# Optimization experiments

Measured on AMD Instinct MI355X. Metric: run time of the kernel, lower is better.

## Reference

```python
import jax, jax.numpy as jnp
import numpy as np
import math

B, S, D, H = 4, 2048, 512, 8
HD = D // H  # head dim = 64

def setup_inputs() -> dict:
    key = jax.random.key(0)
    ks = jax.random.split(key, 12)
    inp = {
        'queries': jax.random.normal(ks[0], (B, S, D), jnp.float32),
        'keys': jax.random.normal(ks[1], (B, S, D), jnp.float32),
        'values': jax.random.normal(ks[2], (B, S, D), jnp.float32),
        'valid_lens': jax.random.randint(ks[3], (B,), 0, 2048, jnp.int32),
        'Wq': jax.random.normal(ks[4], (D, D), jnp.float32) / math.sqrt(D),
        'bq': jnp.zeros((D,), jnp.float32),
        'Wk': jax.random.normal(ks[5], (D, D), jnp.float32) / math.sqrt(D),
        'bk': jnp.zeros((D,), jnp.float32),
        'Wv': jax.random.normal(ks[6], (D, D), jnp.float32) / math.sqrt(D),
        'bv': jnp.zeros((D,), jnp.float32),
        'Wo': jax.random.normal(ks[7], (D, D), jnp.float32) / math.sqrt(D),
        'bo': jnp.zeros((D,), jnp.float32),
    }
    return inp

def reference(queries, keys, values, valid_lens, Wq, bq, Wk, bk, Wv, bv, Wo, bo):
    # project and split heads: [B,S,D] -> [B,H,S,HD]
    def split_heads(x):
        return x.reshape(B, S, H, HD).transpose(0, 2, 1, 3)
    q = split_heads(queries @ Wq + bq)
    k = split_heads(keys @ Wk + bk)
    v = split_heads(values @ Wv + bv)
    # scores [B,H,Sq,Sk]
    scores = jnp.einsum('bhqd,bhkd->bhqk', q, k) / math.sqrt(HD)
    # masked softmax: mask key positions >= valid_len with -1e6 (d2l semantics)
    mask = jnp.arange(S)[None, None, None, :] < valid_lens[:, None, None, None]
    scores = jnp.where(mask, scores, -1e6)
    attn = jax.nn.softmax(scores, axis=-1)
    out = jnp.einsum('bhqk,bhkd->bhqd', attn, v)  # [B,H,S,HD]
    out = out.transpose(0, 2, 1, 3).reshape(B, S, D)
    return out @ Wo + bo
```

## Files before the change

### kernel.cpp

```cpp
#include <hip/hip_runtime.h>
#include <hip/hip_bf16.h>

typedef _Float16 half8 __attribute__((ext_vector_type(8)));
typedef _Float16 half4 __attribute__((ext_vector_type(4)));
typedef float floatx4 __attribute__((ext_vector_type(4)));

#define LOG2E 1.44269504088896340736f

__device__ __forceinline__ half8 cvt8r(floatx4 a, floatx4 b) {
    half8 h;
    h[0] = (_Float16)a[0]; h[1] = (_Float16)a[1]; h[2] = (_Float16)a[2]; h[3] = (_Float16)a[3];
    h[4] = (_Float16)b[0]; h[5] = (_Float16)b[1]; h[6] = (_Float16)b[2]; h[7] = (_Float16)b[3];
    return h;
}

__global__ __launch_bounds__(256) void transpose_w_kernel(
        const float* __restrict__ Wq, const float* __restrict__ Wk,
        const float* __restrict__ Wv, const float* __restrict__ Wo,
        _Float16* __restrict__ out) {
    const float* W = (blockIdx.z == 0) ? Wq : (blockIdx.z == 1) ? Wk : (blockIdx.z == 2) ? Wv : Wo;
    _Float16* o = out + (size_t)blockIdx.z * 512 * 512;
    __shared__ __align__(16) _Float16 t[64][72];
    int r0 = blockIdx.x * 64, c0 = blockIdx.y * 64;
    int tid = threadIdx.x;
    for (int i = 0; i < 2; i++) {
        int f = i * 256 + tid;
        int row = f >> 3, seg = f & 7;
        const float* p = W + (size_t)(r0 + row) * 512 + c0 + seg * 8;
        *(half8*)&t[row][seg * 8] = cvt8r(*(const floatx4*)p, *(const floatx4*)(p + 4));
    }
    __syncthreads();
    for (int i = 0; i < 2; i++) {
        int f = i * 256 + tid;
        int crow = f >> 3, seg = f & 7;
        half8 hv;
        for (int j = 0; j < 8; j++) hv[j] = t[seg * 8 + j][crow];
        *(half8*)(o + (size_t)(c0 + crow) * 512 + r0 + seg * 8) = hv;
    }
}

__global__ __launch_bounds__(256) void gemm_qkv_kernel(
        const float* __restrict__ Xq, const float* __restrict__ Xk, const float* __restrict__ Xv,
        const _Float16* __restrict__ WTall,
        const float* __restrict__ bq, const float* __restrict__ bk, const float* __restrict__ bv,
        _Float16* __restrict__ qo, _Float16* __restrict__ ko2, _Float16* __restrict__ vto) {
    int z = blockIdx.z;
    const float* X = (z == 0) ? Xq : (z == 1) ? Xk : Xv;
    const _Float16* BT = WTall + (size_t)z * 512 * 512;
    const float* bias = (z == 0) ? bq : (z == 1) ? bk : bv;

    __shared__ __align__(16) _Float16 Asm[128][72];
    __shared__ __align__(16) _Float16 Bsm[128][72];

    int tid = threadIdx.x;
    int wave = tid >> 6, lane = tid & 63;
    int lrow = lane & 15, quad = lane >> 4;
    int m0 = (wave >> 1) * 64, n0 = (wave & 1) * 64;
    int mBase = blockIdx.x * 128, nBase = blockIdx.y * 128;

    const floatx4 fz = {0.f, 0.f, 0.f, 0.f};
    floatx4 acc[4][4];
    for (int i = 0; i < 4; i++) for (int j = 0; j < 4; j++) acc[i][j] = fz;

    floatx4 areg[4][2];
    half8 breg[4];
    int srow[4], sseg[4];
    for (int i = 0; i < 4; i++) { int f = i * 256 + tid; srow[i] = f >> 3; sseg[i] = f & 7; }

    for (int i = 0; i < 4; i++) {
        const float* pa = X + (size_t)(mBase + srow[i]) * 512 + sseg[i] * 8;
        areg[i][0] = *(const floatx4*)pa;
        areg[i][1] = *(const floatx4*)(pa + 4);
        breg[i] = *(const half8*)(BT + (size_t)(nBase + srow[i]) * 512 + sseg[i] * 8);
    }

    for (int kb = 0; kb < 512; kb += 64) {
        for (int i = 0; i < 4; i++) {
            *(half8*)&Asm[srow[i]][sseg[i] * 8] = cvt8r(areg[i][0], areg[i][1]);
            *(half8*)&Bsm[srow[i]][sseg[i] * 8] = breg[i];
        }
        __syncthreads();
        if (kb + 64 < 512) {
            int kn = kb + 64;
            for (int i = 0; i < 4; i++) {
                const float* pa = X + (size_t)(mBase + srow[i]) * 512 + kn + sseg[i] * 8;
                areg[i][0] = *(const floatx4*)pa;
                areg[i][1] = *(const floatx4*)(pa + 4);
                breg[i] = *(const half8*)(BT + (size_t)(nBase + srow[i]) * 512 + kn + sseg[i] * 8);
            }
        }
        for (int kc = 0; kc < 2; kc++) {
            int ko_ = kc * 32 + quad * 8;
            half8 a[4], b[4];
            for (int mt = 0; mt < 4; mt++) a[mt] = *(const half8*)&Asm[m0 + mt * 16 + lrow][ko_];
            for (int nt = 0; nt < 4; nt++) b[nt] = *(const half8*)&Bsm[n0 + nt * 16 + lrow][ko_];
            for (int mt = 0; mt < 4; mt++)
                for (int nt = 0; nt < 4; nt++)
                    acc[mt][nt] = __builtin_amdgcn_mfma_f32_16x16x32_f16(a[mt], b[nt], acc[mt][nt], 0, 0, 0);
        }
        __syncthreads();
    }

    if (z == 2) {
        for (int nt = 0; nt < 4; nt++) {
            int gc = nBase + n0 + nt * 16 + lrow;
            float bb = bias[gc];
            int h = gc >> 6, hd = gc & 63;
            for (int mt = 0; mt < 4; mt++) {
                int gr = mBase + m0 + mt * 16 + quad * 4;
                int b_ = gr >> 11, s = gr & 2047;
                half4 hv;
                for (int r = 0; r < 4; r++) hv[r] = (_Float16)(acc[mt][nt][r] + bb);
                *(half4*)(vto + (((size_t)(b_ * 8 + h) * 64 + hd) * 2048 + s)) = hv;
            }
        }
    } else {
        _Float16* out = (z == 0) ? qo : ko2;
        for (int nt = 0; nt < 4; nt++) {
            int gc = nBase + n0 + nt * 16 + lrow;
            float bb = bias[gc];
            int h = gc >> 6, hd = gc & 63;
            for (int mt = 0; mt < 4; mt++) {
                for (int r = 0; r < 4; r++) {
                    int gr = mBase + m0 + mt * 16 + quad * 4 + r;
                    int b_ = gr >> 11, s = gr & 2047;
                    out[(((size_t)b_ * 8 + h) * 2048 + s) * 64 + hd] = (_Float16)(acc[mt][nt][r] + bb);
                }
            }
        }
    }
}

__global__ __launch_bounds__(256) void attn_kernel(
        const _Float16* __restrict__ qws, const _Float16* __restrict__ kws, const _Float16* __restrict__ vtws,
        const int* __restrict__ vlens, _Float16* __restrict__ aout) {
    int idx = blockIdx.x;
    int b = ((idx & 3) + (idx >> 8)) & 3;
    int h = (idx >> 2) & 7;
    int q0 = ((idx >> 5) & 31) * 64;
    int bh = b * 8 + h;
    int L = vlens[b];
    bool uni = (L == 0);
    int nkt = uni ? 32 : ((L + 63) >> 6);
    int tid = threadIdx.x;
    int wave = tid >> 6, lane = tid & 63;
    int lrow = lane & 15, quad = lane >> 4;

    __shared__ __align__(16) _Float16 ksm[64][72];
    __shared__ __align__(16) _Float16 vtsm[80][72];

    for (int i = tid; i < 15 * 36; i += 256) {
        int r = i / 36, c = i % 36;
        ((float*)&vtsm[65 + r][0])[c] = 0.0f;
    }
    if (tid < 64) vtsm[64][tid] = (_Float16)1.0f;

    const _Float16* qbase = qws + ((size_t)bh * 2048 + q0) * 64;
    const _Float16* kbase = kws + (size_t)bh * 2048 * 64;
    const _Float16* vtbase = vtws + (size_t)bh * 64 * 2048;

    half8 qf[2];
    for (int kc = 0; kc < 2; kc++) {
        qf[kc] = *(const half8*)(qbase + (wave * 16 + lrow) * 64 + kc * 32 + quad * 8);
        qf[kc] = qf[kc] * (_Float16)(0.125f * LOG2E);
    }

    const floatx4 fz = {0.f, 0.f, 0.f, 0.f};
    floatx4 oacc[5];
    for (int nt = 0; nt < 5; nt++) oacc[nt] = fz;

    int row0 = tid >> 3, seg = tid & 7;
    half8 kreg[2], vreg[2];
    {
        const _Float16* kt0 = kbase;
        const _Float16* vt0 = vtbase;
        kreg[0] = *(const half8*)(kt0 + tid * 8);
        kreg[1] = *(const half8*)(kt0 + (256 + tid) * 8);
        vreg[0] = *(const half8*)(vt0 + (size_t)row0 * 2048 + seg * 8);
        vreg[1] = *(const half8*)(vt0 + (size_t)(row0 + 32) * 2048 + seg * 8);
    }

    for (int kt = 0; kt < nkt; kt++) {
        *(half8*)&ksm[row0][seg * 8]        = kreg[0];
        *(half8*)&ksm[row0 + 32][seg * 8]   = kreg[1];
        *(half8*)&vtsm[row0][seg * 8]       = vreg[0];
        *(half8*)&vtsm[row0 + 32][seg * 8]  = vreg[1];
        __syncthreads();

        if (kt + 1 < nkt) {
            const _Float16* ktn = kbase + (size_t)(kt + 1) * 64 * 64;
            const _Float16* vtn = vtbase + (kt + 1) * 64;
            kreg[0] = *(const half8*)(ktn + tid * 8);
            kreg[1] = *(const half8*)(ktn + (256 + tid) * 8);
            vreg[0] = *(const half8*)(vtn + (size_t)row0 * 2048 + seg * 8);
            vreg[1] = *(const half8*)(vtn + (size_t)(row0 + 32) * 2048 + seg * 8);
        }

        floatx4 sacc[4];
        for (int km = 0; km < 4; km++) sacc[km] = fz;
        for (int kc = 0; kc < 2; kc++) {
            int ko_ = kc * 32 + quad * 8;
            for (int km = 0; km < 4; km++) {
                half8 kf = *(const half8*)&ksm[km * 16 + lrow][ko_];
                sacc[km] = __builtin_amdgcn_mfma_f32_16x16x32_f16(kf, qf[kc], sacc[km], 0, 0, 0);
            }
        }

        half4 pf[4];
        int kb0 = kt * 64 + quad * 4;
        for (int km = 0; km < 4; km++) {
            int kb = kb0 + km * 16;
            for (int r = 0; r < 4; r++) {
                float p = uni ? 1.0f : ((kb + r < L) ? exp2f(sacc[km][r]) : 0.0f);
                pf[km][r] = (_Float16)p;
            }
        }

        for (int km = 0; km < 4; km++) {
            int kk = km * 16 + quad * 4;
            for (int nt = 0; nt < 5; nt++) {
                half4 bvf = *(const half4*)&vtsm[nt * 16 + lrow][kk];
                oacc[nt] = __builtin_amdgcn_mfma_f32_16x16x16f16(pf[km], bvf, oacc[nt], 0, 0, 0);
            }
        }
        __syncthreads();
    }

    float inv[4];
    for (int r = 0; r < 4; r++)
        inv[r] = 1.0f / __shfl(oacc[4][r], quad << 4, 64);

    for (int nt = 0; nt < 4; nt++) {
        for (int r = 0; r < 4; r++) {
            int s = q0 + wave * 16 + quad * 4 + r;
            aout[((size_t)b * 2048 + s) * 512 + h * 64 + nt * 16 + lrow] =
                (_Float16)(oacc[nt][r] * inv[r]);
        }
    }
}

__global__ __launch_bounds__(256) void gemm_out_kernel(
        const _Float16* __restrict__ A, const _Float16* __restrict__ BT,
        const float* __restrict__ bias, float* __restrict__ out) {
    __shared__ __align__(16) _Float16 Asm[128][72];
    __shared__ __align__(16) _Float16 Bsm[128][72];

    int tid = threadIdx.x;
    int wave = tid >> 6, lane = tid & 63;
    int lrow = lane & 15, quad = lane >> 4;
    int m0 = (wave >> 1) * 64, n0 = (wave & 1) * 64;
    int mBase = blockIdx.x * 128, nBase = blockIdx.y * 128;

    const floatx4 fz = {0.f, 0.f, 0.f, 0.f};
    floatx4 acc[4][4];
    for (int i = 0; i < 4; i++) for (int j = 0; j < 4; j++) acc[i][j] = fz;

    half8 areg[4], breg[4];
    int srow[4], sseg[4];
    for (int i = 0; i < 4; i++) { int f = i * 256 + tid; srow[i] = f >> 3; sseg[i] = f & 7; }
    for (int i = 0; i < 4; i++) {
        areg[i] = *(const half8*)(A + (size_t)(mBase + srow[i]) * 512 + sseg[i] * 8);
        breg[i] = *(const half8*)(BT + (size_t)(nBase + srow[i]) * 512 + sseg[i] * 8);
    }

    for (int kb = 0; kb < 512; kb += 64) {
        for (int i = 0; i < 4; i++) {
            *(half8*)&Asm[srow[i]][sseg[i] * 8] = areg[i];
            *(half8*)&Bsm[srow[i]][sseg[i] * 8] = breg[i];
        }
        __syncthreads();
        if (kb + 64 < 512) {
            int kn = kb + 64;
            for (int i = 0; i < 4; i++) {
                areg[i] = *(const half8*)(A + (size_t)(mBase + srow[i]) * 512 + kn + sseg[i] * 8);
                breg[i] = *(const half8*)(BT + (size_t)(nBase + srow[i]) * 512 + kn + sseg[i] * 8);
            }
        }
        for (int kc = 0; kc < 2; kc++) {
            int ko_ = kc * 32 + quad * 8;
            half8 a[4], b[4];
            for (int mt = 0; mt < 4; mt++) a[mt] = *(const half8*)&Asm[m0 + mt * 16 + lrow][ko_];
            for (int nt = 0; nt < 4; nt++) b[nt] = *(const half8*)&Bsm[n0 + nt * 16 + lrow][ko_];
            for (int mt = 0; mt < 4; mt++)
                for (int nt = 0; nt < 4; nt++)
                    acc[mt][nt] = __builtin_amdgcn_mfma_f32_16x16x32_f16(a[mt], b[nt], acc[mt][nt], 0, 0, 0);
        }
        __syncthreads();
    }

    for (int nt = 0; nt < 4; nt++) {
        int gc = nBase + n0 + nt * 16 + lrow;
        float bb = bias[gc];
        for (int mt = 0; mt < 4; mt++) {
            for (int r = 0; r < 4; r++) {
                int gr = mBase + m0 + mt * 16 + quad * 4 + r;
                out[(size_t)gr * 512 + gc] = acc[mt][nt][r] + bb;
            }
        }
    }
}

extern "C" void kernel_launch(void* const* d_in, const int* in_sizes, int n_in,
                              void* d_out, int out_size, void* d_ws, size_t ws_size,
                              hipStream_t stream) {
    const float* Q  = (const float*)d_in[0];
    const float* K  = (const float*)d_in[1];
    const float* V  = (const float*)d_in[2];
    const int*   VL = (const int*)d_in[3];
    const float* Wq = (const float*)d_in[4];
    const float* bq = (const float*)d_in[5];
    const float* Wk = (const float*)d_in[6];
    const float* bk = (const float*)d_in[7];
    const float* Wv = (const float*)d_in[8];
    const float* bv = (const float*)d_in[9];
    const float* Wo = (const float*)d_in[10];
    const float* bo = (const float*)d_in[11];

    char* ws = (char*)d_ws;
    _Float16* WT   = (_Float16*)ws;
    _Float16* qws  = (_Float16*)(ws + (size_t)(2)  * 1024 * 1024);
    _Float16* kws  = (_Float16*)(ws + (size_t)(10) * 1024 * 1024);
    _Float16* aout = (_Float16*)(ws + (size_t)(18) * 1024 * 1024);
    _Float16* vtws = (_Float16*)(ws + (size_t)(26) * 1024 * 1024);

    transpose_w_kernel<<<dim3(8, 8, 4), 256, 0, stream>>>(Wq, Wk, Wv, Wo, WT);
    gemm_qkv_kernel<<<dim3(64, 4, 3), 256, 0, stream>>>(Q, K, V, WT, bq, bk, bv, qws, kws, vtws);
    attn_kernel<<<dim3(1024, 1, 1), 256, 0, stream>>>(qws, kws, vtws, VL, aout);
    gemm_out_kernel<<<dim3(64, 4, 1), 256, 0, stream>>>(aout, WT + (size_t)3 * 512 * 512, bo, (float*)d_out);
}
```

Measured before the change: 202.0 us.

## Retile GEMMs to 64-row blocks and give attention waves two query tiles

The QKV and output GEMMs switch from 128x128 tiles to 64x128 tiles. Each wave now computes one 16-row strip across all 128 columns, and the grid doubles so more blocks are available. The attention kernel drops to two waves per block, with each wave handling 32 query rows so every K/V fragment read from shared memory feeds two MFMAs. It also adds a mask-free exp path for fully valid key tiles. The costs are higher register pressure in attention, half the waves per block to hide latency, and less operand reuse per wave in the GEMMs.

```diff
diff --git a/kernel.cpp b/kernel.cpp
--- a/kernel.cpp
+++ b/kernel.cpp
@@ -49,89 +49,85 @@
     const _Float16* BT = WTall + (size_t)z * 512 * 512;
     const float* bias = (z == 0) ? bq : (z == 1) ? bk : bv;
 
-    __shared__ __align__(16) _Float16 Asm[128][72];
+    __shared__ __align__(16) _Float16 Asm[64][72];
     __shared__ __align__(16) _Float16 Bsm[128][72];
 
     int tid = threadIdx.x;
     int wave = tid >> 6, lane = tid & 63;
     int lrow = lane & 15, quad = lane >> 4;
-    int m0 = (wave >> 1) * 64, n0 = (wave & 1) * 64;
-    int mBase = blockIdx.x * 128, nBase = blockIdx.y * 128;
+    int mBase = blockIdx.x * 64, nBase = blockIdx.y * 128;
+    int mrow = wave * 16 + lrow;
 
     const floatx4 fz = {0.f, 0.f, 0.f, 0.f};
-    floatx4 acc[4][4];
-    for (int i = 0; i < 4; i++) for (int j = 0; j < 4; j++) acc[i][j] = fz;
-
-    floatx4 areg[4][2];
+    floatx4 acc[8];
+    for (int i = 0; i < 8; i++) acc[i] = fz;
+
+    int arow[2], aseg[2], brow[4], bseg[4];
+    for (int i = 0; i < 2; i++) { int f = i * 256 + tid; arow[i] = f >> 3; aseg[i] = f & 7; }
+    for (int i = 0; i < 4; i++) { int f = i * 256 + tid; brow[i] = f >> 3; bseg[i] = f & 7; }
+
+    floatx4 areg[2][2];
     half8 breg[4];
-    int srow[4], sseg[4];
-    for (int i = 0; i < 4; i++) { int f = i * 256 + tid; srow[i] = f >> 3; sseg[i] = f & 7; }
-
-    for (int i = 0; i < 4; i++) {
-        const float* pa = X + (size_t)(mBase + srow[i]) * 512 + sseg[i] * 8;
+    for (int i = 0; i < 2; i++) {
+        const float* pa = X + (size_t)(mBase + arow[i]) * 512 + aseg[i] * 8;
         areg[i][0] = *(const floatx4*)pa;
         areg[i][1] = *(const floatx4*)(pa + 4);
-        breg[i] = *(const half8*)(BT + (size_t)(nBase + srow[i]) * 512 + sseg[i] * 8);
-    }
+    }
+    for (int i = 0; i < 4; i++)
+        breg[i] = *(const half8*)(BT + (size_t)(nBase + brow[i]) * 512 + bseg[i] * 8);
 
     for (int kb = 0; kb < 512; kb += 64) {
-        for (int i = 0; i < 4; i++) {
-            *(half8*)&Asm[srow[i]][sseg[i] * 8] = cvt8r(areg[i][0], areg[i][1]);
-            *(half8*)&Bsm[srow[i]][sseg[i] * 8] = breg[i];
-        }
+        for (int i = 0; i < 2; i++) *(half8*)&Asm[arow[i]][aseg[i] * 8] = cvt8r(areg[i][0], areg[i][1]);
+        for (int i = 0; i < 4; i++) *(half8*)&Bsm[brow[i]][bseg[i] * 8] = breg[i];
         __syncthreads();
         if (kb + 64 < 512) {
             int kn = kb + 64;
-            for (int i = 0; i < 4; i++) {
-                const float* pa = X + (size_t)(mBase + srow[i]) * 512 + kn + sseg[i] * 8;
+            for (int i = 0; i < 2; i++) {
+                const float* pa = X + (size_t)(mBase + arow[i]) * 512 + kn + aseg[i] * 8;
                 areg[i][0] = *(const floatx4*)pa;
                 areg[i][1] = *(const floatx4*)(pa + 4);
-                breg[i] = *(const half8*)(BT + (size_t)(nBase + srow[i]) * 512 + kn + sseg[i] * 8);
-            }
+            }
+            for (int i = 0; i < 4; i++)
+                breg[i] = *(const half8*)(BT + (size_t)(nBase + brow[i]) * 512 + kn + bseg[i] * 8);
         }
         for (int kc = 0; kc < 2; kc++) {
             int ko_ = kc * 32 + quad * 8;
-            half8 a[4], b[4];
-            for (int mt = 0; mt < 4; mt++) a[mt] = *(const half8*)&Asm[m0 + mt * 16 + lrow][ko_];
-            for (int nt = 0; nt < 4; nt++) b[nt] = *(const half8*)&Bsm[n0 + nt * 16 + lrow][ko_];
-            for (int mt = 0; mt < 4; mt++)
-                for (int nt = 0; nt < 4; nt++)
-                    acc[mt][nt] = __builtin_amdgcn_mfma_f32_16x16x32_f16(a[mt], b[nt], acc[mt][nt], 0, 0, 0);
+            half8 a = *(const half8*)&Asm[mrow][ko_];
+            for (int nt = 0; nt < 8; nt++) {
+                half8 b = *(const half8*)&Bsm[nt * 16 + lrow][ko_];
+                acc[nt] = __builtin_amdgcn_mfma_f32_16x16x32_f16(a, b, acc[nt], 0, 0, 0);
+            }
         }
         __syncthreads();
     }
 
     if (z == 2) {
-        for (int nt = 0; nt < 4; nt++) {
-            int gc = nBase + n0 + nt * 16 + lrow;
+        for (int nt = 0; nt < 8; nt++) {
+            int gc = nBase + nt * 16 + lrow;
             float bb = bias[gc];
             int h = gc >> 6, hd = gc & 63;
-            for (int mt = 0; mt < 4; mt++) {
-                int gr = mBase + m0 + mt * 16 + quad * 4;
-                int b_ = gr >> 11, s = gr & 2047;
-                half4 hv;
-                for (int r = 0; r < 4; r++) hv[r] = (_Float16)(acc[mt][nt][r] + bb);
-                *(half4*)(vto + (((size_t)(b_ * 8 + h) * 64 + hd) * 2048 + s)) = hv;
-            }
+            int gr = mBase + wave * 16 + quad * 4;
+            int b_ = gr >> 11, s = gr & 2047;
+            half4 hv;
+            for (int r = 0; r < 4; r++) hv[r] = (_Float16)(acc[nt][r] + bb);
+            *(half4*)(vto + (((size_t)(b_ * 8 + h) * 64 + hd) * 2048 + s)) = hv;
         }
     } else {
         _Float16* out = (z == 0) ? qo : ko2;
-        for (int nt = 0; nt < 4; nt++) {
-            int gc = nBase + n0 + nt * 16 + lrow;
+        for (int nt = 0; nt < 8; nt++) {
+            int gc = nBase + nt * 16 + lrow;
             float bb = bias[gc];
             int h = gc >> 6, hd = gc & 63;
-            for (int mt = 0; mt < 4; mt++) {
-                for (int r = 0; r < 4; r++) {
-                    int gr = mBase + m0 + mt * 16 + quad * 4 + r;
-                    int b_ = gr >> 11, s = gr & 2047;
-                    out[(((size_t)b_ * 8 + h) * 2048 + s) * 64 + hd] = (_Float16)(acc[mt][nt][r] + bb);
-                }
-            }
-        }
-    }
-}
-
-__global__ __launch_bounds__(256) void attn_kernel(
+            for (int r = 0; r < 4; r++) {
+                int gr = mBase + wave * 16 + quad * 4 + r;
+                int b_ = gr >> 11, s = gr & 2047;
+                out[(((size_t)b_ * 8 + h) * 2048 + s) * 64 + hd] = (_Float16)(acc[nt][r] + bb);
+            }
+        }
+    }
+}
+
+__global__ __launch_bounds__(128) void attn_kernel(
         const _Float16* __restrict__ qws, const _Float16* __restrict__ kws, const _Float16* __restrict__ vtws,
         const int* __restrict__ vlens, _Float16* __restrict__ aout) {
     int idx = blockIdx.x;
@@ -142,14 +138,15 @@
     int L = vlens[b];
     bool uni = (L == 0);
     int nkt = uni ? 32 : ((L + 63) >> 6);
+    int nfull = uni ? 0 : (L >> 6);
     int tid = threadIdx.x;
-    int wave = tid >> 6, lane = tid & 63;
+    int w = tid >> 6, lane = tid & 63;
     int lrow = lane & 15, quad = lane >> 4;
 
     __shared__ __align__(16) _Float16 ksm[64][72];
     __shared__ __align__(16) _Float16 vtsm[80][72];
 
-    for (int i = tid; i < 15 * 36; i += 256) {
+    for (int i = tid; i < 15 * 36; i += 128) {
         int r = i / 36, c = i % 36;
         ((float*)&vtsm[65 + r][0])[c] = 0.0f;
     }
@@ -159,60 +156,66 @@
     const _Float16* kbase = kws + (size_t)bh * 2048 * 64;
     const _Float16* vtbase = vtws + (size_t)bh * 64 * 2048;
 
-    half8 qf[2];
-    for (int kc = 0; kc < 2; kc++) {
-        qf[kc] = *(const half8*)(qbase + (wave * 16 + lrow) * 64 + kc * 32 + quad * 8);
-        qf[kc] = qf[kc] * (_Float16)(0.125f * LOG2E);
-    }
+    half8 qf[2][2];
+    for (int qt = 0; qt < 2; qt++)
+        for (int kc = 0; kc < 2; kc++) {
+            qf[qt][kc] = *(const half8*)(qbase + (w * 32 + qt * 16 + lrow) * 64 + kc * 32 + quad * 8);
+            qf[qt][kc] = qf[qt][kc] * (_Float16)(0.125f * LOG2E);
+        }
 
     const floatx4 fz = {0.f, 0.f, 0.f, 0.f};
-    floatx4 oacc[5];
-    for (int nt = 0; nt < 5; nt++) oacc[nt] = fz;
-
-    int row0 = tid >> 3, seg = tid & 7;
-    half8 kreg[2], vreg[2];
-    {
-        const _Float16* kt0 = kbase;
-        const _Float16* vt0 = vtbase;
-        kreg[0] = *(const half8*)(kt0 + tid * 8);
-        kreg[1] = *(const half8*)(kt0 + (256 + tid) * 8);
-        vreg[0] = *(const half8*)(vt0 + (size_t)row0 * 2048 + seg * 8);
-        vreg[1] = *(const half8*)(vt0 + (size_t)(row0 + 32) * 2048 + seg * 8);
+    floatx4 oacc[2][5];
+    for (int qt = 0; qt < 2; qt++) for (int nt = 0; nt < 5; nt++) oacc[qt][nt] = fz;
+
+    int srow[4], sseg[4];
+    for (int i = 0; i < 4; i++) { int f = i * 128 + tid; srow[i] = f >> 3; sseg[i] = f & 7; }
+    half8 kreg[4], vreg[4];
+    for (int i = 0; i < 4; i++) {
+        kreg[i] = *(const half8*)(kbase + (i * 128 + tid) * 8);
+        vreg[i] = *(const half8*)(vtbase + (size_t)srow[i] * 2048 + sseg[i] * 8);
     }
 
     for (int kt = 0; kt < nkt; kt++) {
-        *(half8*)&ksm[row0][seg * 8]        = kreg[0];
-        *(half8*)&ksm[row0 + 32][seg * 8]   = kreg[1];
-        *(half8*)&vtsm[row0][seg * 8]       = vreg[0];
-        *(half8*)&vtsm[row0 + 32][seg * 8]  = vreg[1];
-        __syncthreads();
-
+        for (int i = 0; i < 4; i++) {
+            *(half8*)&ksm[srow[i]][sseg[i] * 8]  = kreg[i];
+            *(half8*)&vtsm[srow[i]][sseg[i] * 8] = vreg[i];
+        }
+        __syncthreads();
         if (kt + 1 < nkt) {
             const _Float16* ktn = kbase + (size_t)(kt + 1) * 64 * 64;
             const _Float16* vtn = vtbase + (kt + 1) * 64;
-            kreg[0] = *(const half8*)(ktn + tid * 8);
-            kreg[1] = *(const half8*)(ktn + (256 + tid) * 8);
-            vreg[0] = *(const half8*)(vtn + (size_t)row0 * 2048 + seg * 8);
-            vreg[1] = *(const half8*)(vtn + (size_t)(row0 + 32) * 2048 + seg * 8);
-        }
-
-        floatx4 sacc[4];
-        for (int km = 0; km < 4; km++) sacc[km] = fz;
+            for (int i = 0; i < 4; i++) {
+                kreg[i] = *(const half8*)(ktn + (i * 128 + tid) * 8);
+                vreg[i] = *(const half8*)(vtn + (size_t)srow[i] * 2048 + sseg[i] * 8);
+            }
+        }
+
+        floatx4 sacc[2][4];
+        for (int qt = 0; qt < 2; qt++) for (int km = 0; km < 4; km++) sacc[qt][km] = fz;
         for (int kc = 0; kc < 2; kc++) {
             int ko_ = kc * 32 + quad * 8;
             for (int km = 0; km < 4; km++) {
                 half8 kf = *(const half8*)&ksm[km * 16 + lrow][ko_];
-                sacc[km] = __builtin_amdgcn_mfma_f32_16x16x32_f16(kf, qf[kc], sacc[km], 0, 0, 0);
-            }
-        }
-
-        half4 pf[4];
-        int kb0 = kt * 64 + quad * 4;
-        for (int km = 0; km < 4; km++) {
-            int kb = kb0 + km * 16;
-            for (int r = 0; r < 4; r++) {
-                float p = uni ? 1.0f : ((kb + r < L) ? exp2f(sacc[km][r]) : 0.0f);
-                pf[km][r] = (_Float16)p;
+                sacc[0][km] = __builtin_amdgcn_mfma_f32_16x16x32_f16(kf, qf[0][kc], sacc[0][km], 0, 0, 0);
+                sacc[1][km] = __builtin_amdgcn_mfma_f32_16x16x32_f16(kf, qf[1][kc], sacc[1][km], 0, 0, 0);
+            }
+        }
+
+        half4 pf[2][4];
+        if (kt < nfull) {
+            for (int qt = 0; qt < 2; qt++)
+                for (int km = 0; km < 4; km++)
+                    for (int r = 0; r < 4; r++)
+                        pf[qt][km][r] = (_Float16)exp2f(sacc[qt][km][r]);
+        } else {
+            int kb0 = kt * 64 + quad * 4;
+            for (int km = 0; km < 4; km++) {
+                int kb = kb0 + km * 16;
+                for (int qt = 0; qt < 2; qt++)
+                    for (int r = 0; r < 4; r++) {
+                        float p = uni ? 1.0f : ((kb + r < L) ? exp2f(sacc[qt][km][r]) : 0.0f);
+                        pf[qt][km][r] = (_Float16)p;
+                    }
             }
         }
 
@@ -220,21 +223,23 @@
             int kk = km * 16 + quad * 4;
             for (int nt = 0; nt < 5; nt++) {
                 half4 bvf = *(const half4*)&vtsm[nt * 16 + lrow][kk];
-                oacc[nt] = __builtin_amdgcn_mfma_f32_16x16x16f16(pf[km], bvf, oacc[nt], 0, 0, 0);
-            }
-        }
-        __syncthreads();
-    }
-
-    float inv[4];
-    for (int r = 0; r < 4; r++)
-        inv[r] = 1.0f / __shfl(oacc[4][r], quad << 4, 64);
-
-    for (int nt = 0; nt < 4; nt++) {
-        for (int r = 0; r < 4; r++) {
-            int s = q0 + wave * 16 + quad * 4 + r;
-            aout[((size_t)b * 2048 + s) * 512 + h * 64 + nt * 16 + lrow] =
-                (_Float16)(oacc[nt][r] * inv[r]);
+                oacc[0][nt] = __builtin_amdgcn_mfma_f32_16x16x16f16(pf[0][km], bvf, oacc[0][nt], 0, 0, 0);
+                oacc[1][nt] = __builtin_amdgcn_mfma_f32_16x16x16f16(pf[1][km], bvf, oacc[1][nt], 0, 0, 0);
+            }
+        }
+        __syncthreads();
+    }
+
+    for (int qt = 0; qt < 2; qt++) {
+        float inv[4];
+        for (int r = 0; r < 4; r++)
+            inv[r] = 1.0f / __shfl(oacc[qt][4][r], quad << 4, 64);
+        for (int nt = 0; nt < 4; nt++) {
+            for (int r = 0; r < 4; r++) {
+                int s = q0 + w * 32 + qt * 16 + quad * 4 + r;
+                aout[((size_t)b * 2048 + s) * 512 + h * 64 + nt * 16 + lrow] =
+                    (_Float16)(oacc[qt][nt][r] * inv[r]);
+            }
         }
     }
 }
@@ -242,60 +247,57 @@
 __global__ __launch_bounds__(256) void gemm_out_kernel(
         const _Float16* __restrict__ A, const _Float16* __restrict__ BT,
         const float* __restrict__ bias, float* __restrict__ out) {
-    __shared__ __align__(16) _Float16 Asm[128][72];
+    __shared__ __align__(16) _Float16 Asm[64][72];
     __shared__ __align__(16) _Float16 Bsm[128][72];
 
     int tid = threadIdx.x;
     int wave = tid >> 6, lane = tid & 63;
     int lrow = lane & 15, quad = lane >> 4;
-    int m0 = (wave >> 1) * 64, n0 = (wave & 1) * 64;
-    int mBase = blockIdx.x * 128, nBase = blockIdx.y * 128;
+    int mBase = blockIdx.x * 64, nBase = blockIdx.y * 128;
+    int mrow = wave * 16 + lrow;
 
     const floatx4 fz = {0.f, 0.f, 0.f, 0.f};
-    floatx4 acc[4][4];
-    for (int i = 0; i < 4; i++) for (int j = 0; j < 4; j++) acc[i][j] = fz;
-
-    half8 areg[4], breg[4];
-    int srow[4], sseg[4];
-    for (int i = 0; i < 4; i++) { int f = i * 256 + tid; srow[i] = f >> 3; sseg[i] = f & 7; }
-    for (int i = 0; i < 4; i++) {
-        areg[i] = *(const half8*)(A + (size_t)(mBase + srow[i]) * 512 + sseg[i] * 8);
-        breg[i] = *(const half8*)(BT + (size_t)(nBase + srow[i]) * 512 + sseg[i] * 8);
-    }
+    floatx4 acc[8];
+    for (int i = 0; i < 8; i++) acc[i] = fz;
+
+    int arow[2], aseg[2], brow[4], bseg[4];
+    for (int i = 0; i < 2; i++) { int f = i * 256 + tid; arow[i] = f >> 3; aseg[i] = f & 7; }
+    for (int i = 0; i < 4; i++) { int f = i * 256 + tid; brow[i] = f >> 3; bseg[i] = f & 7; }
+
+    half8 areg[2], breg[4];
+    for (int i = 0; i < 2; i++)
+        areg[i] = *(const half8*)(A + (size_t)(mBase + arow[i]) * 512 + aseg[i] * 8);
+    for (int i = 0; i < 4; i++)
+        breg[i] = *(const half8*)(BT + (size_t)(nBase + brow[i]) * 512 + bseg[i] * 8);
 
     for (int kb = 0; kb < 512; kb += 64) {
-        for (int i = 0; i < 4; i++) {
-            *(half8*)&Asm[srow[i]][sseg[i] * 8] = areg[i];
-            *(half8*)&Bsm[srow[i]][sseg[i] * 8] = breg[i];
-        }
+        for (int i = 0; i < 2; i++) *(half8*)&Asm[arow[i]][aseg[i] * 8] = areg[i];
+        for (int i = 0; i < 4; i++) *(half8*)&Bsm[brow[i]][bseg[i] * 8] = breg[i];
         __syncthreads();
         if (kb + 64 < 512) {
             int kn = kb + 64;
-            for (int i = 0; i < 4; i++) {
-                areg[i] = *(const half8*)(A + (size_t)(mBase + srow[i]) * 512 + kn + sseg[i] * 8);
-                breg[i] = *(const half8*)(BT + (size_t)(nBase + srow[i]) * 512 + kn + sseg[i] * 8);
-            }
+            for (int i = 0; i < 2; i++)
+                areg[i] = *(const half8*)(A + (size_t)(mBase + arow[i]) * 512 + kn + aseg[i] * 8);
+            for (int i = 0; i < 4; i++)
+                breg[i] = *(const half8*)(BT + (size_t)(nBase + brow[i]) * 512 + kn + bseg[i] * 8);
         }
         for (int kc = 0; kc < 2; kc++) {
             int ko_ = kc * 32 + quad * 8;
-            half8 a[4], b[4];
-            for (int mt = 0; mt < 4; mt++) a[mt] = *(const half8*)&Asm[m0 + mt * 16 + lrow][ko_];
-            for (int nt = 0; nt < 4; nt++) b[nt] = *(const half8*)&Bsm[n0 + nt * 16 + lrow][ko_];
-            for (int mt = 0; mt < 4; mt++)
-                for (int nt = 0; nt < 4; nt++)
-                    acc[mt][nt] = __builtin_amdgcn_mfma_f32_16x16x32_f16(a[mt], b[nt], acc[mt][nt], 0, 0, 0);
-        }
-        __syncthreads();
-    }
-
-    for (int nt = 0; nt < 4; nt++) {
-        int gc = nBase + n0 + nt * 16 + lrow;
+            half8 a = *(const half8*)&Asm[mrow][ko_];
+            for (int nt = 0; nt < 8; nt++) {
+                half8 b = *(const half8*)&Bsm[nt * 16 + lrow][ko_];
+                acc[nt] = __builtin_amdgcn_mfma_f32_16x16x32_f16(a, b, acc[nt], 0, 0, 0);
+            }
+        }
+        __syncthreads();
+    }
+
+    for (int nt = 0; nt < 8; nt++) {
+        int gc = nBase + nt * 16 + lrow;
         float bb = bias[gc];
-        for (int mt = 0; mt < 4; mt++) {
-            for (int r = 0; r < 4; r++) {
-                int gr = mBase + m0 + mt * 16 + quad * 4 + r;
-                out[(size_t)gr * 512 + gc] = acc[mt][nt][r] + bb;
-            }
+        for (int r = 0; r < 4; r++) {
+            int gr = mBase + wave * 16 + quad * 4 + r;
+            out[(size_t)gr * 512 + gc] = acc[nt][r] + bb;
         }
     }
 }
@@ -324,7 +326,7 @@
     _Float16* vtws = (_Float16*)(ws + (size_t)(26) * 1024 * 1024);
 
     transpose_w_kernel<<<dim3(8, 8, 4), 256, 0, stream>>>(Wq, Wk, Wv, Wo, WT);
-    gemm_qkv_kernel<<<dim3(64, 4, 3), 256, 0, stream>>>(Q, K, V, WT, bq, bk, bv, qws, kws, vtws);
-    attn_kernel<<<dim3(1024, 1, 1), 256, 0, stream>>>(qws, kws, vtws, VL, aout);
-    gemm_out_kernel<<<dim3(64, 4, 1), 256, 0, stream>>>(aout, WT + (size_t)3 * 512 * 512, bo, (float*)d_out);
-}
+    gemm_qkv_kernel<<<dim3(128, 4, 3), 256, 0, stream>>>(Q, K, V, WT, bq, bk, bv, qws, kws, vtws);
+    attn_kernel<<<dim3(1024, 1, 1), 128, 0, stream>>>(qws, kws, vtws, VL, aout);
+    gemm_out_kernel<<<dim3(128, 4, 1), 256, 0, stream>>>(aout, WT + (size_t)3 * 512 * 512, bo, (float*)d_out);
+}
```

Result: faster. 194.1 us (-3.9%).
